# Kernel optimization log

Hardware: AMD Instinct MI355X
Metric: run time of the kernel (lower is better)

The kernel has to match this reference:

```python
import jax, jax.numpy as jnp
import numpy as np

EMBED_DIM = 1024
NUM_HEADS = 16
HEAD_DIM = EMBED_DIM // NUM_HEADS
SCALING_FACTOR = 0.1
SCALING = (HEAD_DIM * SCALING_FACTOR) ** (-0.5)
B, L = 4, 1024


def setup_inputs() -> dict:
    key = jax.random.key(0)
    ks = jax.random.split(key, 8)
    query = jax.random.normal(ks[0], (B, L, EMBED_DIM), dtype=jnp.float32)
    key_padding_mask = jnp.zeros((B, L), dtype=bool)
    attn_bias = jax.random.normal(ks[1], (B * NUM_HEADS, L, L), dtype=jnp.float32)
    s_in = 1.0 / np.sqrt(EMBED_DIM)
    Wqkv = jax.random.normal(ks[2], (3 * EMBED_DIM, EMBED_DIM), dtype=jnp.float32) * s_in
    bqkv = jnp.zeros((3 * EMBED_DIM,), dtype=jnp.float32)
    Wo = jax.random.normal(ks[3], (EMBED_DIM, EMBED_DIM), dtype=jnp.float32) * s_in
    bo = jnp.zeros((EMBED_DIM,), dtype=jnp.float32)
    return {"query": query, "key_padding_mask": key_padding_mask, "attn_bias": attn_bias,
            "Wqkv": Wqkv, "bqkv": bqkv, "Wo": Wo, "bo": bo}


def reference(query, key_padding_mask, attn_bias, Wqkv, bqkv, Wo, bo):
    b, l, e = query.shape
    # fused in-projection: (B, L, 3E)
    qkv = jnp.einsum("ble,fe->blf", query, Wqkv) + bqkv
    q, k, v = jnp.split(qkv, 3, axis=-1)
    q = q * SCALING
    # (B, L, H, D)
    q = q.reshape(b, l, NUM_HEADS, HEAD_DIM)
    k = k.reshape(b, l, NUM_HEADS, HEAD_DIM)
    v = v.reshape(b, l, NUM_HEADS, HEAD_DIM)
    # scores: (B, H, L, L)
    scores = jnp.einsum("blhd,bmhd->bhlm", q, k)
    scores = scores + attn_bias.reshape(b, NUM_HEADS, l, l)
    neg_inf = jnp.asarray(-jnp.inf, scores.dtype)
    scores = jnp.where(key_padding_mask[:, None, None, :], neg_inf, scores)
    probs = jax.nn.softmax(scores, axis=-1)  # dropout: eval mode (identity)
    out = jnp.einsum("bhlm,bmhd->blhd", probs, v).reshape(b, l, e)
    return jnp.einsum("ble,fe->blf", out, Wo) + bo
```

## Files before the change

kernel.cpp:

```cpp
#include <hip/hip_runtime.h>
#include <math.h>

#define EMB   1024
#define NH    16
#define HD    64
#define BATCH 4
#define LSEQ  1024
#define NTOK  (BATCH*LSEQ)
#define SCALING 0.39528470752104744f

typedef __attribute__((ext_vector_type(8))) short short8;
typedef __attribute__((ext_vector_type(4))) float f32x4;

__device__ __forceinline__ float bf2f(short s) {
    union { float f; unsigned u; } x; x.u = ((unsigned)(unsigned short)s) << 16; return x.f;
}
__device__ __forceinline__ short f2bf(float f) {
    union { float f; unsigned u; } x; x.f = f;
    unsigned r = x.u + 0x7fff + ((x.u >> 16) & 1);
    return (short)(r >> 16);
}

__device__ __forceinline__ void glds16(const void* g, void* l) {
    __builtin_amdgcn_global_load_lds(
        (const __attribute__((address_space(1))) void*)g,
        (__attribute__((address_space(3))) void*)l, 16, 0, 0);
}

#define QCHUNKS  (4096*1024/8)
#define WCHUNKS  (3072*1024/8)
#define WOCHUNKS (1024*1024/8)
__global__ __launch_bounds__(256) void cvt_all(
    const float* __restrict__ q, const float* __restrict__ wqkv,
    const float* __restrict__ wo,
    short* __restrict__ xb, short* __restrict__ wb, short* __restrict__ wob)
{
    int c = blockIdx.x * 256 + threadIdx.x;
    const float* src; short* dst; int off;
    if (c < QCHUNKS)                { src = q;    dst = xb;  off = c; }
    else if (c < QCHUNKS + WCHUNKS) { src = wqkv; dst = wb;  off = c - QCHUNKS; }
    else                            { src = wo;   dst = wob; off = c - QCHUNKS - WCHUNKS; }
    int i = off * 8;
    float4 a = *(const float4*)(src + i);
    float4 b = *(const float4*)(src + i + 4);
    short8 o;
    o[0] = f2bf(a.x); o[1] = f2bf(a.y); o[2] = f2bf(a.z); o[3] = f2bf(a.w);
    o[4] = f2bf(b.x); o[5] = f2bf(b.y); o[6] = f2bf(b.z); o[7] = f2bf(b.w);
    *(short8*)(dst + i) = o;
}

__global__ __launch_bounds__(256) void qkv_gemm(
    const short* __restrict__ X, const short* __restrict__ W,
    const float* __restrict__ bqkv,
    short* __restrict__ qws, short* __restrict__ kws, short* __restrict__ vws)
{
    __shared__ short As[128 * 32];
    __shared__ short Bs[128 * 32];
    const int tid = threadIdx.x;
    const int wave = tid >> 6, lane = tid & 63;
    const int quad = lane >> 4, l16 = lane & 15;
    const int m0 = blockIdx.y * 128, n0 = blockIdx.x * 128;
    const int wm = (wave >> 1) * 64, wn = (wave & 1) * 64;

    f32x4 acc[4][4] = {};

    const int srow = wave * 16 + (lane >> 2);
    const int scol = (lane & 3) * 16;

    const char* gA = (const char*)X + (size_t)(m0 + srow) * 2048 + scol;
    const char* gB = (const char*)W + (size_t)(n0 + srow) * 2048 + scol;
    char* lA = (char*)As + wave * 1024 + lane * 16;
    char* lB = (char*)Bs + wave * 1024 + lane * 16;

    for (int kt = 0; kt < 1024; kt += 32) {
        __syncthreads();
        const char* ga = gA + kt * 2;
        const char* gb = gB + kt * 2;
        glds16(ga, lA);
        glds16(ga + (size_t)64 * 2048, lA + 4096);
        glds16(gb, lB);
        glds16(gb + (size_t)64 * 2048, lB + 4096);
        __syncthreads();

        short8 af[4], bf[4];
        #pragma unroll
        for (int i = 0; i < 4; i++)
            af[i] = *(const short8*)((const char*)As + (wm + i * 16 + l16) * 64 + quad * 16);
        #pragma unroll
        for (int j = 0; j < 4; j++)
            bf[j] = *(const short8*)((const char*)Bs + (wn + j * 16 + l16) * 64 + quad * 16);
        #pragma unroll
        for (int i = 0; i < 4; i++)
            #pragma unroll
            for (int j = 0; j < 4; j++)
                acc[i][j] = __builtin_amdgcn_mfma_f32_16x16x32_bf16(af[i], bf[j], acc[i][j], 0, 0, 0);
    }

    #pragma unroll
    for (int i = 0; i < 4; i++) {
        #pragma unroll
        for (int j = 0; j < 4; j++) {
            #pragma unroll
            for (int r = 0; r < 4; r++) {
                int gm = m0 + wm + i * 16 + quad * 4 + r;
                int gn = n0 + wn + j * 16 + l16;
                float v = acc[i][j][r] + bqkv[gn];
                int part = gn >> 10;
                int cc = gn & 1023;
                int h = cc >> 6, d = cc & 63;
                int b = gm >> 10, l = gm & 1023;
                size_t dst = (((size_t)(b * NH + h)) * LSEQ + l) * HD + d;
                if (part == 0)      qws[dst] = f2bf(v * SCALING);
                else if (part == 1) kws[dst] = f2bf(v);
                else                vws[dst] = f2bf(v);
            }
        }
    }
}

__global__ __launch_bounds__(256, 3) void attn_kernel(
    const short* __restrict__ qws, const short* __restrict__ kws,
    const short* __restrict__ vws, const float* __restrict__ bias,
    const unsigned char* __restrict__ mask, short* __restrict__ att)
{
    __shared__ short Ks[128 * 64];
    __shared__ short Vt[64 * 136];
    __shared__ short Ps[4 * 16 * 136];

    const int qt = blockIdx.x;
    const int bh = blockIdx.y;
    const int b = bh >> 4;
    const int tid = threadIdx.x, wave = tid >> 6, lane = tid & 63;
    const int quad = lane >> 4, l16 = lane & 15;

    const short* Qg = qws + (size_t)bh * LSEQ * HD + (size_t)qt * 64 * HD;
    const short* Kg = kws + (size_t)bh * LSEQ * HD;
    const short* Vg = vws + (size_t)bh * LSEQ * HD;
    const float* Bg = bias + (size_t)bh * LSEQ * LSEQ;

    short8 qf[2];
    #pragma unroll
    for (int ks = 0; ks < 2; ks++)
        qf[ks] = *(const short8*)(Qg + (wave * 16 + l16) * HD + ks * 32 + quad * 8);

    float m_r[4], l_r[4];
    f32x4 o[4] = {};
    #pragma unroll
    for (int r = 0; r < 4; r++) { m_r[r] = -INFINITY; l_r[r] = 0.0f; }

    const int qrow_g = qt * 64 + wave * 16 + quad * 4;
    const float* Bp = Bg + (size_t)qrow_g * LSEQ + l16;
    const unsigned char* Mp = mask + (size_t)b * LSEQ + l16;

    for (int kt0 = 0; kt0 < LSEQ; kt0 += 128) {
        float bv[8][4];
        #pragma unroll
        for (int ni = 0; ni < 8; ni++)
            #pragma unroll
            for (int r = 0; r < 4; r++)
                bv[ni][r] = Bp[(size_t)r * LSEQ + kt0 + ni * 16];
        unsigned char mk[8];
        #pragma unroll
        for (int ni = 0; ni < 8; ni++) mk[ni] = Mp[kt0 + ni * 16];
        short8 vst[4];
        #pragma unroll
        for (int i = 0; i < 4; i++) {
            int c = i * 256 + tid;
            int row = c >> 3, c8 = c & 7;
            vst[i] = *(const short8*)(Vg + (size_t)(kt0 + row) * HD + c8 * 8);
        }

        __syncthreads();

        #pragma unroll
        for (int i = 0; i < 4; i++) {
            int c = i * 256 + tid;
            int row = c >> 3;
            int u = (c & 7) ^ (row & 7);
            glds16((const char*)Kg + (size_t)(kt0 + row) * 128 + u * 16,
                   (char*)Ks + c * 16);
        }
        #pragma unroll
        for (int i = 0; i < 4; i++) {
            int c = i * 256 + tid;
            int row = c >> 3, c8 = c & 7;
            int rl = row & 7, ru = row >> 3;
            #pragma unroll
            for (int j = 0; j < 8; j++) {
                int d = c8 * 8 + j;
                Vt[d * 136 + ((ru ^ c8) & 15) * 8 + rl] = vst[i][j];
            }
        }
        __syncthreads();

        f32x4 s[8] = {};
        #pragma unroll
        for (int ni = 0; ni < 8; ni++) {
            int krow = ni * 16 + l16;
            #pragma unroll
            for (int ks = 0; ks < 2; ks++) {
                int u = (ks * 4 + quad) ^ (krow & 7);
                short8 kf = *(const short8*)((const char*)Ks + krow * 128 + u * 16);
                s[ni] = __builtin_amdgcn_mfma_f32_16x16x32_bf16(qf[ks], kf, s[ni], 0, 0, 0);
            }
        }

        #pragma unroll
        for (int ni = 0; ni < 8; ni++) {
            #pragma unroll
            for (int r = 0; r < 4; r++) {
                float val = s[ni][r] + bv[ni][r];
                s[ni][r] = mk[ni] ? -INFINITY : val;
            }
        }

        #pragma unroll
        for (int r = 0; r < 4; r++) {
            float mx = s[0][r];
            #pragma unroll
            for (int ni = 1; ni < 8; ni++) mx = fmaxf(mx, s[ni][r]);
            #pragma unroll
            for (int off = 1; off < 16; off <<= 1)
                mx = fmaxf(mx, __shfl_xor(mx, off, 64));
            float mnew = fmaxf(m_r[r], mx);
            float alpha = (m_r[r] == -INFINITY) ? 0.0f : __expf(m_r[r] - mnew);
            m_r[r] = mnew;
            float sum = 0.0f;
            #pragma unroll
            for (int ni = 0; ni < 8; ni++) {
                float p = __expf(s[ni][r] - mnew);
                s[ni][r] = p;
                sum += p;
            }
            #pragma unroll
            for (int off = 1; off < 16; off <<= 1)
                sum += __shfl_xor(sum, off, 64);
            l_r[r] = l_r[r] * alpha + sum;
            #pragma unroll
            for (int ni2 = 0; ni2 < 4; ni2++) o[ni2][r] *= alpha;
            #pragma unroll
            for (int ni = 0; ni < 8; ni++)
                Ps[wave * 2176 + (quad * 4 + r) * 136 + ni * 16 + l16] = f2bf(s[ni][r]);
        }

        #pragma unroll
        for (int ks = 0; ks < 4; ks++) {
            short8 pf = *(const short8*)((const char*)Ps + wave * 4352 + l16 * 272 + ks * 64 + quad * 16);
            #pragma unroll
            for (int ni2 = 0; ni2 < 4; ni2++) {
                int d = ni2 * 16 + l16;
                int u = (ks * 4 + quad) ^ ((d >> 3) & 7);
                short8 vf = *(const short8*)((const char*)Vt + d * 272 + u * 16);
                o[ni2] = __builtin_amdgcn_mfma_f32_16x16x32_bf16(pf, vf, o[ni2], 0, 0, 0);
            }
        }
    }

    const int h = bh & 15;
    #pragma unroll
    for (int r = 0; r < 4; r++) {
        float inv = 1.0f / l_r[r];
        int lq = qt * 64 + wave * 16 + quad * 4 + r;
        #pragma unroll
        for (int ni2 = 0; ni2 < 4; ni2++) {
            int d = ni2 * 16 + l16;
            att[((size_t)(b * LSEQ + lq)) * EMB + h * HD + d] = f2bf(o[ni2][r] * inv);
        }
    }
}

__global__ __launch_bounds__(256) void out_gemm(
    const short* __restrict__ Xa, const short* __restrict__ Wo,
    const float* __restrict__ bo, float* __restrict__ out)
{
    __shared__ short As[128 * 32];
    __shared__ short Bs[64 * 32];
    const int tid = threadIdx.x;
    const int wave = tid >> 6, lane = tid & 63;
    const int quad = lane >> 4, l16 = lane & 15;
    const int m0 = blockIdx.y * 128, n0 = blockIdx.x * 64;
    const int wm = (wave >> 1) * 64, wn = (wave & 1) * 32;

    f32x4 acc[4][2] = {};

    const int srow = wave * 16 + (lane >> 2);
    const int scol = (lane & 3) * 16;
    const char* gA = (const char*)Xa + (size_t)(m0 + srow) * 2048 + scol;
    const char* gB = (const char*)Wo + (size_t)(n0 + (tid >> 2)) * 2048 + (tid & 3) * 16;
    char* lA = (char*)As + wave * 1024 + lane * 16;
    char* lB = (char*)Bs + tid * 16;

    for (int kt = 0; kt < 1024; kt += 32) {
        __syncthreads();
        const char* ga = gA + kt * 2;
        glds16(ga, lA);
        glds16(ga + (size_t)64 * 2048, lA + 4096);
        glds16(gB + kt * 2, lB);
        __syncthreads();

        short8 af[4], bf[2];
        #pragma unroll
        for (int i = 0; i < 4; i++)
            af[i] = *(const short8*)((const char*)As + (wm + i * 16 + l16) * 64 + quad * 16);
        #pragma unroll
        for (int j = 0; j < 2; j++)
            bf[j] = *(const short8*)((const char*)Bs + (wn + j * 16 + l16) * 64 + quad * 16);
        #pragma unroll
        for (int i = 0; i < 4; i++)
            #pragma unroll
            for (int j = 0; j < 2; j++)
                acc[i][j] = __builtin_amdgcn_mfma_f32_16x16x32_bf16(af[i], bf[j], acc[i][j], 0, 0, 0);
    }

    #pragma unroll
    for (int i = 0; i < 4; i++) {
        #pragma unroll
        for (int j = 0; j < 2; j++) {
            #pragma unroll
            for (int r = 0; r < 4; r++) {
                int gm = m0 + wm + i * 16 + quad * 4 + r;
                int gn = n0 + wn + j * 16 + l16;
                out[(size_t)gm * EMB + gn] = acc[i][j][r] + bo[gn];
            }
        }
    }
}

extern "C" void kernel_launch(void* const* d_in, const int* in_sizes, int n_in,
                              void* d_out, int out_size, void* d_ws, size_t ws_size,
                              hipStream_t stream) {
    const float* query = (const float*)d_in[0];
    const unsigned char* mask = (const unsigned char*)d_in[1];
    const float* bias = (const float*)d_in[2];
    const float* Wqkv = (const float*)d_in[3];
    const float* bqkv = (const float*)d_in[4];
    const float* Wo   = (const float*)d_in[5];
    const float* bo   = (const float*)d_in[6];
    float* out = (float*)d_out;

    short* Xb  = (short*)d_ws;
    short* Wb  = Xb  + (size_t)4096 * 1024;
    short* Wob = Wb  + (size_t)3072 * 1024;
    short* qws = Wob + (size_t)1024 * 1024;
    short* kws = qws + (size_t)64 * 1024 * 64;
    short* vws = kws + (size_t)64 * 1024 * 64;
    short* att = vws + (size_t)64 * 1024 * 64;

    cvt_all<<<dim3((QCHUNKS + WCHUNKS + WOCHUNKS) / 256), 256, 0, stream>>>(
        query, Wqkv, Wo, Xb, Wb, Wob);

    qkv_gemm<<<dim3(24, 32), 256, 0, stream>>>(Xb, Wb, bqkv, qws, kws, vws);
    attn_kernel<<<dim3(16, 64), 256, 0, stream>>>(qws, kws, vws, bias, mask, att);
    out_gemm<<<dim3(16, 32), 256, 0, stream>>>(att, Wob, bo, out);
}
```

Baseline: 482.3 us.

## Double GEMM K-tile with XOR-swizzled LDS; alias K and P buffers in attention

Both projection GEMMs now stage a 64-wide K slice per iteration, with an XOR swizzle on the LDS layout. This halves the number of barrier pairs and reduces LDS bank conflicts. The attention kernel aliases the probability tile onto the K buffer, which cuts LDS use so the launch bound can allow four blocks per CU. It prefetches the next V tile during the PV stage and moves the bias loads after the barrier. The buffer aliasing adds an extra __syncthreads per iteration and raises register pressure under the tighter occupancy target.

Result: slower. 539.4 us (+11.8%).

```diff
diff --git a/kernel.cpp b/kernel.cpp
--- a/kernel.cpp
+++ b/kernel.cpp
@@ -54,8 +54,8 @@
     const float* __restrict__ bqkv,
     short* __restrict__ qws, short* __restrict__ kws, short* __restrict__ vws)
 {
-    __shared__ short As[128 * 32];
-    __shared__ short Bs[128 * 32];
+    __shared__ short As[128 * 64];
+    __shared__ short Bs[128 * 64];
     const int tid = threadIdx.x;
     const int wave = tid >> 6, lane = tid & 63;
     const int quad = lane >> 4, l16 = lane & 15;
@@ -64,36 +64,39 @@
 
     f32x4 acc[4][4] = {};
 
-    const int srow = wave * 16 + (lane >> 2);
-    const int scol = (lane & 3) * 16;
-
-    const char* gA = (const char*)X + (size_t)(m0 + srow) * 2048 + scol;
-    const char* gB = (const char*)W + (size_t)(n0 + srow) * 2048 + scol;
-    char* lA = (char*)As + wave * 1024 + lane * 16;
-    char* lB = (char*)Bs + wave * 1024 + lane * 16;
-
-    for (int kt = 0; kt < 1024; kt += 32) {
-        __syncthreads();
-        const char* ga = gA + kt * 2;
-        const char* gb = gB + kt * 2;
-        glds16(ga, lA);
-        glds16(ga + (size_t)64 * 2048, lA + 4096);
-        glds16(gb, lB);
-        glds16(gb + (size_t)64 * 2048, lB + 4096);
-        __syncthreads();
-
-        short8 af[4], bf[4];
-        #pragma unroll
-        for (int i = 0; i < 4; i++)
-            af[i] = *(const short8*)((const char*)As + (wm + i * 16 + l16) * 64 + quad * 16);
-        #pragma unroll
-        for (int j = 0; j < 4; j++)
-            bf[j] = *(const short8*)((const char*)Bs + (wn + j * 16 + l16) * 64 + quad * 16);
-        #pragma unroll
-        for (int i = 0; i < 4; i++)
+    const int srow = tid >> 3;
+    const int sx   = (tid & 7) ^ ((tid >> 3) & 7);
+    const char* gA = (const char*)X + (size_t)(m0 + srow) * 2048 + sx * 16;
+    const char* gB = (const char*)W + (size_t)(n0 + srow) * 2048 + sx * 16;
+    char* lA = (char*)As + tid * 16;
+    char* lB = (char*)Bs + tid * 16;
+    const int rx = l16 & 7;
+
+    for (int kt = 0; kt < 1024; kt += 64) {
+        __syncthreads();
+        #pragma unroll
+        for (int p = 0; p < 4; p++) {
+            glds16(gA + (size_t)(p * 32) * 2048 + kt * 2, lA + p * 4096);
+            glds16(gB + (size_t)(p * 32) * 2048 + kt * 2, lB + p * 4096);
+        }
+        __syncthreads();
+
+        #pragma unroll
+        for (int kk = 0; kk < 2; kk++) {
+            const int u = (kk * 4 + quad) ^ rx;
+            short8 af[4], bf[4];
+            #pragma unroll
+            for (int i = 0; i < 4; i++)
+                af[i] = *(const short8*)((const char*)As + (wm + i * 16 + l16) * 128 + u * 16);
             #pragma unroll
             for (int j = 0; j < 4; j++)
-                acc[i][j] = __builtin_amdgcn_mfma_f32_16x16x32_bf16(af[i], bf[j], acc[i][j], 0, 0, 0);
+                bf[j] = *(const short8*)((const char*)Bs + (wn + j * 16 + l16) * 128 + u * 16);
+            #pragma unroll
+            for (int i = 0; i < 4; i++)
+                #pragma unroll
+                for (int j = 0; j < 4; j++)
+                    acc[i][j] = __builtin_amdgcn_mfma_f32_16x16x32_bf16(af[i], bf[j], acc[i][j], 0, 0, 0);
+        }
     }
 
     #pragma unroll
@@ -118,14 +121,13 @@
     }
 }
 
-__global__ __launch_bounds__(256, 3) void attn_kernel(
+__global__ __launch_bounds__(256, 4) void attn_kernel(
     const short* __restrict__ qws, const short* __restrict__ kws,
     const short* __restrict__ vws, const float* __restrict__ bias,
     const unsigned char* __restrict__ mask, short* __restrict__ att)
 {
-    __shared__ short Ks[128 * 64];
+    __shared__ short KP[8448];
     __shared__ short Vt[64 * 136];
-    __shared__ short Ps[4 * 16 * 136];
 
     const int qt = blockIdx.x;
     const int bh = blockIdx.y;
@@ -152,24 +154,14 @@
     const float* Bp = Bg + (size_t)qrow_g * LSEQ + l16;
     const unsigned char* Mp = mask + (size_t)b * LSEQ + l16;
 
+    short8 vst[4];
+    #pragma unroll
+    for (int i = 0; i < 4; i++) {
+        int c = i * 256 + tid;
+        vst[i] = *(const short8*)(Vg + (size_t)(c >> 3) * HD + (c & 7) * 8);
+    }
+
     for (int kt0 = 0; kt0 < LSEQ; kt0 += 128) {
-        float bv[8][4];
-        #pragma unroll
-        for (int ni = 0; ni < 8; ni++)
-            #pragma unroll
-            for (int r = 0; r < 4; r++)
-                bv[ni][r] = Bp[(size_t)r * LSEQ + kt0 + ni * 16];
-        unsigned char mk[8];
-        #pragma unroll
-        for (int ni = 0; ni < 8; ni++) mk[ni] = Mp[kt0 + ni * 16];
-        short8 vst[4];
-        #pragma unroll
-        for (int i = 0; i < 4; i++) {
-            int c = i * 256 + tid;
-            int row = c >> 3, c8 = c & 7;
-            vst[i] = *(const short8*)(Vg + (size_t)(kt0 + row) * HD + c8 * 8);
-        }
-
         __syncthreads();
 
         #pragma unroll
@@ -178,7 +170,7 @@
             int row = c >> 3;
             int u = (c & 7) ^ (row & 7);
             glds16((const char*)Kg + (size_t)(kt0 + row) * 128 + u * 16,
-                   (char*)Ks + c * 16);
+                   (char*)KP + c * 16);
         }
         #pragma unroll
         for (int i = 0; i < 4; i++) {
@@ -193,6 +185,16 @@
         }
         __syncthreads();
 
+        float bv[8][4];
+        #pragma unroll
+        for (int ni = 0; ni < 8; ni++)
+            #pragma unroll
+            for (int r = 0; r < 4; r++)
+                bv[ni][r] = Bp[(size_t)r * LSEQ + kt0 + ni * 16];
+        unsigned char mk[8];
+        #pragma unroll
+        for (int ni = 0; ni < 8; ni++) mk[ni] = Mp[kt0 + ni * 16];
+
         f32x4 s[8] = {};
         #pragma unroll
         for (int ni = 0; ni < 8; ni++) {
@@ -200,7 +202,7 @@
             #pragma unroll
             for (int ks = 0; ks < 2; ks++) {
                 int u = (ks * 4 + quad) ^ (krow & 7);
-                short8 kf = *(const short8*)((const char*)Ks + krow * 128 + u * 16);
+                short8 kf = *(const short8*)((const char*)KP + krow * 128 + u * 16);
                 s[ni] = __builtin_amdgcn_mfma_f32_16x16x32_bf16(qf[ks], kf, s[ni], 0, 0, 0);
             }
         }
@@ -213,6 +215,8 @@
                 s[ni][r] = mk[ni] ? -INFINITY : val;
             }
         }
+
+        __syncthreads();
 
         #pragma unroll
         for (int r = 0; r < 4; r++) {
@@ -240,12 +244,19 @@
             for (int ni2 = 0; ni2 < 4; ni2++) o[ni2][r] *= alpha;
             #pragma unroll
             for (int ni = 0; ni < 8; ni++)
-                Ps[wave * 2176 + (quad * 4 + r) * 136 + ni * 16 + l16] = f2bf(s[ni][r]);
+                KP[wave * 2112 + (quad * 4 + r) * 132 + ni * 16 + l16] = f2bf(s[ni][r]);
+        }
+
+        int ktn = (kt0 + 128) & (LSEQ - 1);
+        #pragma unroll
+        for (int i = 0; i < 4; i++) {
+            int c = i * 256 + tid;
+            vst[i] = *(const short8*)(Vg + (size_t)(ktn + (c >> 3)) * HD + (c & 7) * 8);
         }
 
         #pragma unroll
         for (int ks = 0; ks < 4; ks++) {
-            short8 pf = *(const short8*)((const char*)Ps + wave * 4352 + l16 * 272 + ks * 64 + quad * 16);
+            short8 pf = *(const short8*)((const char*)KP + wave * 4224 + l16 * 264 + ks * 64 + quad * 16);
             #pragma unroll
             for (int ni2 = 0; ni2 < 4; ni2++) {
                 int d = ni2 * 16 + l16;
@@ -273,8 +284,8 @@
     const short* __restrict__ Xa, const short* __restrict__ Wo,
     const float* __restrict__ bo, float* __restrict__ out)
 {
-    __shared__ short As[128 * 32];
-    __shared__ short Bs[64 * 32];
+    __shared__ short As[128 * 64];
+    __shared__ short Bs[64 * 64];
     const int tid = threadIdx.x;
     const int wave = tid >> 6, lane = tid & 63;
     const int quad = lane >> 4, l16 = lane & 15;
@@ -283,33 +294,40 @@
 
     f32x4 acc[4][2] = {};
 
-    const int srow = wave * 16 + (lane >> 2);
-    const int scol = (lane & 3) * 16;
-    const char* gA = (const char*)Xa + (size_t)(m0 + srow) * 2048 + scol;
-    const char* gB = (const char*)Wo + (size_t)(n0 + (tid >> 2)) * 2048 + (tid & 3) * 16;
-    char* lA = (char*)As + wave * 1024 + lane * 16;
+    const int srow = tid >> 3;
+    const int sx   = (tid & 7) ^ ((tid >> 3) & 7);
+    const char* gA = (const char*)Xa + (size_t)(m0 + srow) * 2048 + sx * 16;
+    const char* gB = (const char*)Wo + (size_t)(n0 + srow) * 2048 + sx * 16;
+    char* lA = (char*)As + tid * 16;
     char* lB = (char*)Bs + tid * 16;
-
-    for (int kt = 0; kt < 1024; kt += 32) {
-        __syncthreads();
-        const char* ga = gA + kt * 2;
-        glds16(ga, lA);
-        glds16(ga + (size_t)64 * 2048, lA + 4096);
-        glds16(gB + kt * 2, lB);
-        __syncthreads();
-
-        short8 af[4], bf[2];
-        #pragma unroll
-        for (int i = 0; i < 4; i++)
-            af[i] = *(const short8*)((const char*)As + (wm + i * 16 + l16) * 64 + quad * 16);
-        #pragma unroll
-        for (int j = 0; j < 2; j++)
-            bf[j] = *(const short8*)((const char*)Bs + (wn + j * 16 + l16) * 64 + quad * 16);
-        #pragma unroll
-        for (int i = 0; i < 4; i++)
+    const int rx = l16 & 7;
+
+    for (int kt = 0; kt < 1024; kt += 64) {
+        __syncthreads();
+        #pragma unroll
+        for (int p = 0; p < 4; p++)
+            glds16(gA + (size_t)(p * 32) * 2048 + kt * 2, lA + p * 4096);
+        #pragma unroll
+        for (int p = 0; p < 2; p++)
+            glds16(gB + (size_t)(p * 32) * 2048 + kt * 2, lB + p * 4096);
+        __syncthreads();
+
+        #pragma unroll
+        for (int kk = 0; kk < 2; kk++) {
+            const int u = (kk * 4 + quad) ^ rx;
+            short8 af[4], bf[2];
+            #pragma unroll
+            for (int i = 0; i < 4; i++)
+                af[i] = *(const short8*)((const char*)As + (wm + i * 16 + l16) * 128 + u * 16);
             #pragma unroll
             for (int j = 0; j < 2; j++)
-                acc[i][j] = __builtin_amdgcn_mfma_f32_16x16x32_bf16(af[i], bf[j], acc[i][j], 0, 0, 0);
+                bf[j] = *(const short8*)((const char*)Bs + (wn + j * 16 + l16) * 128 + u * 16);
+            #pragma unroll
+            for (int i = 0; i < 4; i++)
+                #pragma unroll
+                for (int j = 0; j < 2; j++)
+                    acc[i][j] = __builtin_amdgcn_mfma_f32_16x16x32_bf16(af[i], bf[j], acc[i][j], 0, 0, 0);
+        }
     }
 
     #pragma unroll
```
